# Optimization experiments

Hardware: AMD Instinct MI355X
Metric: run time of the kernel (lower is better)

The kernel has to match this reference:

```python
import jax, jax.numpy as jnp
import numpy as np

G = 8192          # graphs in batch
A = 5             # num_agents (nodes per graph)
N = G * A         # total nodes
IN_CH = 29
HID = 64
HEADS = 8
D = HID * HEADS   # 512, node/graph feature dim
NOPT = 4
ADIM = 3


def _lin(key, fan_in, fan_out):
    return jax.random.normal(key, (fan_in, fan_out), jnp.float32) / np.sqrt(fan_in)


def setup_inputs() -> dict:
    key = jax.random.key(0)
    ks = jax.random.split(key, 40)
    # --- graph structure: G fully-connected 5-node graphs + self loops ---
    pairs = np.array([(i, j) for i in range(A) for j in range(A) if i != j])  # [20,2]
    base = (np.arange(G)[:, None] * A)
    src = (base + pairs[None, :, 0]).reshape(-1)
    dst = (base + pairs[None, :, 1]).reshape(-1)
    # GATConv adds self loops (fill_value=0.0 for edge_attr)
    loop = np.arange(N)
    edge_src = jnp.asarray(np.concatenate([src, loop]), jnp.int32)
    edge_dst = jnp.asarray(np.concatenate([dst, loop]), jnp.int32)
    e_real = jax.random.uniform(ks[0], (src.shape[0], 1), jnp.float32)
    edge_attr = jnp.concatenate([e_real, jnp.zeros((N, 1), jnp.float32)], axis=0)
    batch_map = jnp.asarray(np.repeat(np.arange(G), A), jnp.int32)
    x = jax.random.normal(ks[1], (N, IN_CH), jnp.float32)
    sc = 1.0 / np.sqrt(HID)
    inp = dict(
        x=x, edge_attr=edge_attr, edge_src=edge_src, edge_dst=edge_dst, batch_map=batch_map,
        # conv1
        W1=_lin(ks[2], IN_CH, D), as1=jax.random.normal(ks[3], (HEADS, HID)) * sc,
        ad1=jax.random.normal(ks[4], (HEADS, HID)) * sc, We1=_lin(ks[5], 1, D),
        ae1=jax.random.normal(ks[6], (HEADS, HID)) * sc, b1=jnp.zeros((D,), jnp.float32),
        # conv2
        W2=_lin(ks[7], D, D), as2=jax.random.normal(ks[8], (HEADS, HID)) * sc,
        ad2=jax.random.normal(ks[9], (HEADS, HID)) * sc, We2=_lin(ks[10], 1, D),
        ae2=jax.random.normal(ks[11], (HEADS, HID)) * sc, b2=jnp.zeros((D,), jnp.float32),
        # policy-over-options head
        pw1=_lin(ks[12], D, 2 * HID), pb1=jnp.zeros((2 * HID,)), pw2=_lin(ks[13], 2 * HID, NOPT), pb2=jnp.zeros((NOPT,)),
        # q-options head
        qw1=_lin(ks[14], D, 2 * HID), qb1=jnp.zeros((2 * HID,)), qw2=_lin(ks[15], 2 * HID, NOPT), qb2=jnp.zeros((NOPT,)),
        # intra-option actor head (option 0), input dim = node + graph feature = 2*D
        aw1=_lin(ks[16], 2 * D, 2 * HID), ab1=jnp.zeros((2 * HID,)), aw2=_lin(ks[17], 2 * HID, 2 * ADIM), ab2=jnp.zeros((2 * ADIM,)),
        # termination head (option 0)
        tw1=_lin(ks[18], D, HID), tb1=jnp.zeros((HID,)), tw2=_lin(ks[19], HID, 1), tb2=jnp.zeros((1,)),
        action_limits=jnp.array([1.0, 1.0, 3.14159], jnp.float32),
    )
    return inp


def _gat(x, src, dst, eattr, W, a_s, a_d, We, a_e, b):
    n = x.shape[0]
    h = (x @ W).reshape(n, HEADS, HID)                      # [N,H,C]
    e = (eattr @ We).reshape(-1, HEADS, HID)                # [E,H,C]
    lg = ((h * a_s).sum(-1)[src] + (h * a_d).sum(-1)[dst]
          + (e * a_e).sum(-1))                              # [E,H]
    lg = jnp.where(lg > 0, lg, 0.2 * lg)                    # leaky_relu(0.2)
    m = jax.ops.segment_max(lg, dst, num_segments=n)
    p = jnp.exp(lg - m[dst])
    denom = jax.ops.segment_sum(p, dst, num_segments=n)[dst] + 1e-16
    alpha = p / denom                                       # scatter-softmax over dst
    out = jax.ops.segment_sum(alpha[:, :, None] * h[src], dst, num_segments=n)
    return out.reshape(n, HEADS * HID) + b


def reference(x, edge_attr, edge_src, edge_dst, batch_map,
              W1, as1, ad1, We1, ae1, b1,
              W2, as2, ad2, We2, ae2, b2,
              pw1, pb1, pw2, pb2, qw1, qb1, qw2, qb2,
              aw1, ab1, aw2, ab2, tw1, tb1, tw2, tb2, action_limits):
    h = jax.nn.relu(_gat(x, edge_src, edge_dst, edge_attr, W1, as1, ad1, We1, ae1, b1))
    h = jax.nn.relu(_gat(h, edge_src, edge_dst, edge_attr, W2, as2, ad2, We2, ae2, b2))
    # global_mean_pool
    cnt = jax.ops.segment_sum(jnp.ones((h.shape[0],), h.dtype), batch_map, num_segments=G)
    g = jax.ops.segment_sum(h, batch_map, num_segments=G) / cnt[:, None]   # [G,D]
    pi = jax.nn.relu(g @ pw1 + pb1) @ pw2 + pb2                            # [G,NOPT]
    q = jax.nn.relu(g @ qw1 + qb1) @ qw2 + qb2                             # [G,NOPT]
    term = jax.nn.sigmoid(jax.nn.relu(g @ tw1 + tb1) @ tw2 + tb2)          # [G,1]
    # per-graph first num_agents nodes == all nodes here (5 per graph)
    agent = h.reshape(G, A, D)
    comb = jnp.concatenate([agent, jnp.broadcast_to(g[:, None, :], (G, A, D))], axis=-1)
    ho = jax.nn.relu(comb @ aw1 + ab1) @ aw2 + ab2                          # [G,A,6]
    mean_raw, log_std_raw = jnp.split(ho, 2, axis=-1)
    mean = jnp.tanh(mean_raw) * action_limits                               # [G,A,3]
    std = 0.05 + jax.nn.sigmoid(log_std_raw) * 0.45 + 1e-6
    return jnp.concatenate([pi, q, term, mean.reshape(G, -1), std.reshape(G, -1)], axis=1)
```

## Files before the change

### kernel.cpp

```cpp
#include <hip/hip_runtime.h>
#include <hip/hip_bf16.h>
#include <math.h>

#define GG 8192
#define AA 5
#define NN (GG * AA)
#define DD 512

typedef unsigned short ushort_t;
typedef unsigned int uint_t;

__device__ inline float bf2f(ushort_t u) {
  union { uint_t i; float f; } c; c.i = ((uint_t)u) << 16; return c.f;
}
__device__ inline ushort_t f2bf(float f) {
  union { float f; uint_t i; } c; c.f = f;
  uint_t r = c.i + 0x7fffu + ((c.i >> 16) & 1u);
  return (ushort_t)(r >> 16);
}

using frag8 = __attribute__((ext_vector_type(8))) short;
using f32x4 = __attribute__((ext_vector_type(4))) float;

typedef __attribute__((address_space(3))) void lds_void;
typedef __attribute__((address_space(1))) const void gbl_void;
#define GLL(g, l) __builtin_amdgcn_global_load_lds((gbl_void*)(g), (lds_void*)(l), 16, 0, 0)

__device__ inline int xcd_swz(int bid, int nwg) {
  return (bid & 7) * (nwg >> 3) + (bid >> 3);
}

__global__ __launch_bounds__(256) void k_prep(
    const float* __restrict__ x, const float* __restrict__ W1,
    const float* __restrict__ W2, const float* __restrict__ pw1,
    const float* __restrict__ qw1, const float* __restrict__ tw1,
    const float* __restrict__ aw1, const float* __restrict__ pb1,
    const float* __restrict__ qb1, const float* __restrict__ tb1,
    const float* __restrict__ ab1, const float* __restrict__ We1,
    const float* __restrict__ ae1, const float* __restrict__ We2,
    const float* __restrict__ ae2, const float* __restrict__ as1,
    const float* __restrict__ ad1, const float* __restrict__ as2,
    const float* __restrict__ ad2, const float* __restrict__ pw2,
    const float* __restrict__ pb2, const float* __restrict__ qw2,
    const float* __restrict__ qb2, const float* __restrict__ tw2,
    const float* __restrict__ tb2, const float* __restrict__ aw2,
    const float* __restrict__ ab2, ushort_t* __restrict__ xpad32,
    ushort_t* __restrict__ W1T32, ushort_t* __restrict__ W2T,
    ushort_t* __restrict__ WcatT, ushort_t* __restrict__ aw1topT,
    ushort_t* __restrict__ wsc1T, ushort_t* __restrict__ wsc2T,
    float* __restrict__ bcat, float* __restrict__ sce,
    float* __restrict__ woutT, float* __restrict__ bout) {
  int b = blockIdx.x;
  int t = threadIdx.x;
  if (b < 1024) {
    int i = b * 256 + t;
    int n = i >> 9, k = i & 511;
    W2T[(size_t)n * 512 + k] = f2bf(W2[(size_t)k * 512 + n]);
    float v;
    if (n < 128)      v = pw1[(size_t)k * 128 + n];
    else if (n < 256) v = qw1[(size_t)k * 128 + (n - 128)];
    else if (n < 320) v = tw1[(size_t)k * 64 + (n - 256)];
    else if (n < 448) v = aw1[(size_t)(512 + k) * 128 + (n - 320)];
    else              v = 0.f;
    WcatT[(size_t)n * 512 + k] = f2bf(v);
    if (n < 128) aw1topT[(size_t)n * 512 + k] = f2bf(aw1[(size_t)k * 128 + n]);
    if (k == 0) {
      float bv;
      if (n < 128)      bv = pb1[n];
      else if (n < 256) bv = qb1[n - 128];
      else if (n < 320) bv = tb1[n - 256];
      else if (n < 448) bv = ab1[n - 320];
      else              bv = 0.f;
      bcat[n] = bv;
    }
    if (i < 512 * 32) {
      int nn = i >> 5, kk = i & 31;
      W1T32[i] = (kk < 29) ? f2bf(W1[(size_t)kk * 512 + nn]) : (ushort_t)0;
    }
    if (i < 16384) {
      int k2 = i & 511, srow = i >> 9;
      int nh2 = srow >> 4, s = srow & 15;
      float val = 0.f;
      if (s < 8) {
        int head = nh2 * 4 + (s >> 1);
        const float* av = ((s & 1) ? ad2 : as2) + head * 64;
        const float* wr = W2 + (size_t)k2 * 512 + head * 64;
        for (int c = 0; c < 64; ++c) val = fmaf(wr[c], av[c], val);
      }
      wsc2T[i] = f2bf(val);
    }
    if (i < 1024) {
      int k1 = i & 31, srow = i >> 5;
      int nh1 = srow >> 4, s = srow & 15;
      float val = 0.f;
      if (s < 8 && k1 < 29) {
        int head = nh1 * 4 + (s >> 1);
        const float* av = ((s & 1) ? ad1 : as1) + head * 64;
        const float* wr = W1 + (size_t)k1 * 512 + head * 64;
        for (int c = 0; c < 64; ++c) val = fmaf(wr[c], av[c], val);
      }
      wsc1T[i] = f2bf(val);
    }
    if (i < 16) {
      int h = i & 7;
      const float* Wp = (i < 8) ? We1 : We2;
      const float* ap = (i < 8) ? ae1 : ae2;
      float c = 0.f;
      for (int k2 = 0; k2 < 64; ++k2) c = fmaf(Wp[h * 64 + k2], ap[h * 64 + k2], c);
      sce[i] = c;
    }
    if (i < 5120) {
      int j = i / 40, o = i % 40;
      float wv;
      if (o < 4)       wv = pw2[j * 4 + o];
      else if (o < 8)  wv = qw2[j * 4 + (o - 4)];
      else if (o == 8) wv = (j < 64) ? tw2[j] : 0.f;
      else if (o < 24) wv = aw2[j * 6 + (o - 9) % 3];
      else if (o < 39) wv = aw2[j * 6 + 3 + (o - 24) % 3];
      else             wv = 0.f;
      woutT[i] = wv;
      if (j == 0) {
        float bv;
        if (o < 4)       bv = pb2[o];
        else if (o < 8)  bv = qb2[o - 4];
        else if (o == 8) bv = tb2[0];
        else if (o < 24) bv = ab2[(o - 9) % 3];
        else if (o < 39) bv = ab2[3 + (o - 24) % 3];
        else             bv = 0.f;
        bout[o] = bv;
      }
    }
  } else {
    int i = (b - 1024) * 256 + t;
    int n = i >> 5, k = i & 31;
    xpad32[i] = (k < 29) ? f2bf(x[(size_t)n * 29 + k]) : (ushort_t)0;
  }
}

template <int KDIM, bool POOL>
__global__ __launch_bounds__(512) void k_fused(
    const ushort_t* __restrict__ A, const ushort_t* __restrict__ BT,
    const ushort_t* __restrict__ WS, const float* __restrict__ eattr,
    const float* __restrict__ sce, const float* __restrict__ bvec,
    ushort_t* __restrict__ hout, ushort_t* __restrict__ gmean) {
  __shared__ __align__(16) char smem[51200];
  const int t = threadIdx.x;
  const int lane = t & 63;
  const int w = t >> 6;
  const int l15 = lane & 15;
  const int ko2 = ((((lane >> 4) ^ (lane & 3) ^ ((lane >> 2) & 3)) & 3) * 16);
  int lid = xcd_swz(blockIdx.x, gridDim.x);
  const int mb = lid >> 1, nh = lid & 1;
  const int m0 = mb * 80;
  const int g0 = mb * 16;
  const int n0 = nh * 256;
  const ushort_t* WSn = WS + (size_t)nh * 16 * KDIM;
  constexpr int nt = KDIM / 32;
  f32x4 acc[5][2] = {};
  f32x4 asc[5] = {};
  float* sal = (float*)(smem + 42240);
  float* sss = (float*)(smem + 48640);
  float* ssd = (float*)(smem + 49920);
#define FSTAGE(bi, kk0)                                                        \
  {                                                                            \
    char* bb_ = smem + (bi) * 16384;                                           \
    char* aa_ = smem + 32768 + (bi) * 5120;                                    \
    char* sb_ = smem + 43008 + (bi) * 1024;                                    \
    _Pragma("unroll")                                                          \
    for (int r_ = 0; r_ < 2; ++r_) {                                           \
      int c_ = t + r_ * 512; int row_ = c_ >> 2;                               \
      int sw_ = ((((c_ & 3) ^ (row_ & 3) ^ ((row_ >> 2) & 3)) & 3)) * 8;       \
      GLL(BT + (size_t)(n0 + row_) * KDIM + (kk0) + sw_, bb_ + c_ * 16);       \
    }                                                                          \
    if (t < 320) {                                                             \
      int c_ = t; int row_ = c_ >> 2;                                          \
      int sw_ = ((((c_ & 3) ^ (row_ & 3) ^ ((row_ >> 2) & 3)) & 3)) * 8;       \
      GLL(A + (size_t)(m0 + row_) * KDIM + (kk0) + sw_, aa_ + c_ * 16);        \
    } else if (t < 384) {                                                      \
      int c_ = t - 320; int row_ = c_ >> 2;                                    \
      int sw_ = ((((c_ & 3) ^ (row_ & 3) ^ ((row_ >> 2) & 3)) & 3)) * 8;       \
      GLL(WSn + (size_t)row_ * KDIM + (kk0) + sw_, sb_ + c_ * 16);             \
    }                                                                          \
  }
  FSTAGE(0, 0);
  for (int ts = 0; ts < nt; ++ts) {
    int cur = ts & 1;
    if (ts + 1 < nt) {
      FSTAGE(cur ^ 1, (ts + 1) * 32);
      if (w < 6) { asm volatile("s_waitcnt vmcnt(3)" ::: "memory"); }
      else       { asm volatile("s_waitcnt vmcnt(2)" ::: "memory"); }
    } else {
      asm volatile("s_waitcnt vmcnt(0)" ::: "memory");
    }
    __builtin_amdgcn_s_barrier();
    __builtin_amdgcn_sched_barrier(0);
    const char* bb = smem + cur * 16384;
    const char* aa = smem + 32768 + cur * 5120;
    const char* sb = smem + 43008 + cur * 1024;
    frag8 af[5], bfr[2];
#pragma unroll
    for (int mt = 0; mt < 5; ++mt)
      af[mt] = *(const frag8*)(aa + (mt * 16 + l15) * 64 + ko2);
#pragma unroll
    for (int n = 0; n < 2; ++n)
      bfr[n] = *(const frag8*)(bb + ((2 * w + n) * 16 + l15) * 64 + ko2);
    __builtin_amdgcn_s_setprio(1);
#pragma unroll
    for (int mt = 0; mt < 5; ++mt)
#pragma unroll
      for (int n = 0; n < 2; ++n)
        acc[mt][n] = __builtin_amdgcn_mfma_f32_16x16x32_bf16(af[mt], bfr[n], acc[mt][n], 0, 0, 0);
    if (w == 7) {
      frag8 sfr = *(const frag8*)(sb + l15 * 64 + ko2);
#pragma unroll
      for (int mt = 0; mt < 5; ++mt)
        asc[mt] = __builtin_amdgcn_mfma_f32_16x16x32_bf16(af[mt], sfr, asc[mt], 0, 0, 0);
    }
    __builtin_amdgcn_s_setprio(0);
    __builtin_amdgcn_sched_barrier(0);
    if (ts == nt - 1 && w == 7 && l15 < 8) {
      float* dst = (lane & 1) ? ssd : sss;
      int hd = l15 >> 1;
      int q4 = (lane >> 4) * 4;
#pragma unroll
      for (int mt = 0; mt < 5; ++mt)
#pragma unroll
        for (int r = 0; r < 4; ++r)
          dst[(mt * 16 + q4 + r) * 4 + hd] = asc[mt][r];
    }
    __builtin_amdgcn_s_barrier();
  }
#undef FSTAGE
  float* hbf = (float*)smem;
  {
    if (w < 4) {
      int q4 = (lane >> 4) * 4;
#pragma unroll
      for (int mt = 0; mt < 5; ++mt)
#pragma unroll
        for (int n = 0; n < 2; ++n) {
          int lc = w * 32 + n * 16 + l15;
#pragma unroll
          for (int r = 0; r < 4; ++r)
            hbf[(mt * 16 + q4 + r) * 132 + lc] = acc[mt][n][r];
        }
    } else if (t - 256 < 160) {
      int u = t - 256;
      int gi = u / 10, jh = u % 10;
      int j = jh >> 1, hd0 = jh & 1;
#pragma unroll
      for (int hh = 0; hh < 2; ++hh) {
        int hd = hd0 + hh * 2;
        int g = g0 + gi;
        float sdj = ssd[(gi * 5 + j) * 4 + hd];
        float ce = sce[nh * 4 + hd];
        float lg[5], mx = -1e30f;
#pragma unroll
        for (int i = 0; i < 5; ++i) {
          float l = sss[(gi * 5 + i) * 4 + hd] + sdj;
          if (i != j) l = fmaf(eattr[(size_t)g * 20 + i * 4 + (j > i ? j - 1 : j)], ce, l);
          l = l > 0.f ? l : 0.2f * l;
          lg[i] = l; mx = fmaxf(mx, l);
        }
        float s = 0.f;
#pragma unroll
        for (int i = 0; i < 5; ++i) { lg[i] = __expf(lg[i] - mx); s += lg[i]; }
        float inv = 1.f / (s + 1e-16f);
#pragma unroll
        for (int i = 0; i < 5; ++i) sal[((gi * 5 + j) * 5 + i) * 4 + hd] = lg[i] * inv;
      }
    }
  }
  __syncthreads();
#pragma unroll
  for (int half = 0; half < 2; ++half) {
    if (half == 1) {
      if (w >= 4) {
        int q4 = (lane >> 4) * 4;
#pragma unroll
        for (int mt = 0; mt < 5; ++mt)
#pragma unroll
          for (int n = 0; n < 2; ++n) {
            int lc = (w - 4) * 32 + n * 16 + l15;
#pragma unroll
            for (int r = 0; r < 4; ++r)
              hbf[(mt * 16 + q4 + r) * 132 + lc] = acc[mt][n][r];
          }
      }
      __syncthreads();
    }
    int gi = t >> 5, cq = t & 31;
    int hd = half * 2 + (cq >> 4);
    int colg = n0 + half * 128 + cq * 4;
    float hv[5][4];
#pragma unroll
    for (int i = 0; i < 5; ++i)
      *(float4*)hv[i] = *(const float4*)&hbf[(gi * 5 + i) * 132 + cq * 4];
    float4 bb4 = *(const float4*)&bvec[colg];
    float gs0 = 0.f, gs1 = 0.f, gs2 = 0.f, gs3 = 0.f;
#pragma unroll
    for (int j = 0; j < 5; ++j) {
      float o0 = bb4.x, o1 = bb4.y, o2 = bb4.z, o3 = bb4.w;
#pragma unroll
      for (int i = 0; i < 5; ++i) {
        float a = sal[((gi * 5 + j) * 5 + i) * 4 + hd];
        o0 = fmaf(a, hv[i][0], o0); o1 = fmaf(a, hv[i][1], o1);
        o2 = fmaf(a, hv[i][2], o2); o3 = fmaf(a, hv[i][3], o3);
      }
      o0 = fmaxf(o0, 0.f); o1 = fmaxf(o1, 0.f);
      o2 = fmaxf(o2, 0.f); o3 = fmaxf(o3, 0.f);
      uint2 wv_;
      wv_.x = (uint_t)f2bf(o0) | ((uint_t)f2bf(o1) << 16);
      wv_.y = (uint_t)f2bf(o2) | ((uint_t)f2bf(o3) << 16);
      *(uint2*)(hout + ((size_t)(g0 + gi) * 5 + j) * 512 + colg) = wv_;
      if (POOL) { gs0 += o0; gs1 += o1; gs2 += o2; gs3 += o3; }
    }
    if (POOL) {
      uint2 wv_;
      wv_.x = (uint_t)f2bf(gs0 * 0.2f) | ((uint_t)f2bf(gs1 * 0.2f) << 16);
      wv_.y = (uint_t)f2bf(gs2 * 0.2f) | ((uint_t)f2bf(gs3 * 0.2f) << 16);
      *(uint2*)(gmean + (size_t)(g0 + gi) * 512 + colg) = wv_;
    }
    if (half == 0) __syncthreads();
  }
}

template <int EPI>
__device__ __forceinline__ void gemm_body(
    const ushort_t* __restrict__ A, const ushort_t* __restrict__ BT,
    const float* __restrict__ bias, void* __restrict__ Cv,
    int M, int N, int K, int m0, int n0, char* lds) {
  int t = threadIdx.x;
  int lane = t & 63;
  int wv = t >> 6;
  int wr = (wv >> 1) * 64, wc = (wv & 1) * 64;
  f32x4 acc[4][4] = {};
  int ch0 = t, ch1 = t + 256;
  int row0 = ch0 >> 2, row1 = ch1 >> 2;
  int sw0 = (((ch0 & 3) ^ (row0 & 3) ^ ((row0 >> 2) & 3)) & 3) * 8;
  int sw1 = (((ch1 & 3) ^ (row1 & 3) ^ ((row1 >> 2) & 3)) & 3) * 8;
  int ko2 = ((((lane >> 4) ^ (lane & 3) ^ ((lane >> 2) & 3)) & 3) * 16);
  const int nt = K >> 5;
#define STAGE(bi, kk0)                                                         \
  {                                                                            \
    char* ab = lds + (bi) * 16384;                                             \
    GLL(A + (size_t)(m0 + row0) * K + (kk0) + sw0, ab + ch0 * 16);             \
    GLL(A + (size_t)(m0 + row1) * K + (kk0) + sw1, ab + ch1 * 16);             \
    GLL(BT + (size_t)(n0 + row0) * K + (kk0) + sw0, ab + 8192 + ch0 * 16);     \
    GLL(BT + (size_t)(n0 + row1) * K + (kk0) + sw1, ab + 8192 + ch1 * 16);     \
  }
  STAGE(0, 0);
  if (nt > 1) STAGE(1, 32);
  for (int ts = 0; ts < nt; ++ts) {
    int bi = ts % 3;
    if (ts + 2 < nt) {
      STAGE((ts + 2) % 3, (ts + 2) * 32);
      asm volatile("s_waitcnt vmcnt(8)" ::: "memory");
    } else if (ts + 1 < nt) {
      asm volatile("s_waitcnt vmcnt(4)" ::: "memory");
    } else {
      asm volatile("s_waitcnt vmcnt(0)" ::: "memory");
    }
    __builtin_amdgcn_s_barrier();
    __builtin_amdgcn_sched_barrier(0);
    const char* ab = lds + bi * 16384;
    frag8 af[4], bfr[4];
#pragma unroll
    for (int m = 0; m < 4; ++m)
      af[m] = *(const frag8*)(ab + (wr + m * 16 + (lane & 15)) * 64 + ko2);
#pragma unroll
    for (int n = 0; n < 4; ++n)
      bfr[n] = *(const frag8*)(ab + 8192 + (wc + n * 16 + (lane & 15)) * 64 + ko2);
#pragma unroll
    for (int m = 0; m < 4; ++m)
#pragma unroll
      for (int n = 0; n < 4; ++n)
        acc[m][n] = __builtin_amdgcn_mfma_f32_16x16x32_bf16(af[m], bfr[n], acc[m][n], 0, 0, 0);
    __builtin_amdgcn_sched_barrier(0);
    __builtin_amdgcn_s_barrier();
  }
#undef STAGE
  int r4 = (lane >> 4) * 4;
  int cl = lane & 15;
#pragma unroll
  for (int m = 0; m < 4; ++m) {
#pragma unroll
    for (int n = 0; n < 4; ++n) {
      int col = n0 + wc + n * 16 + cl;
      float bb = (EPI == 2) ? bias[col] : 0.f;
#pragma unroll
      for (int r = 0; r < 4; ++r) {
        int row = m0 + wr + m * 16 + r4 + r;
        float v = acc[m][n][r] + bb;
        if (EPI == 2 && col < 320) v = fmaxf(v, 0.f);
        ((float*)Cv)[(size_t)row * N + col] = v;
      }
    }
  }
}

__global__ __launch_bounds__(256) void k_hgemm(
    const ushort_t* __restrict__ h2, const ushort_t* __restrict__ aw1topT,
    float* __restrict__ ahid, const ushort_t* __restrict__ gmean,
    const ushort_t* __restrict__ WcatT, const float* __restrict__ bcat,
    float* __restrict__ hcat) {
  __shared__ char lds[49152];
  int bid = blockIdx.x;
  if (bid < 320) {
    int lid = xcd_swz(bid, 320);
    gemm_body<1>(h2, aw1topT, nullptr, ahid, NN, 128, DD, lid * 128, 0, lds);
  } else {
    int lid = xcd_swz(bid - 320, 256);
    gemm_body<2>(gmean, WcatT, bcat, hcat, GG, DD, DD, (lid >> 2) * 128, (lid & 3) * 128, lds);
  }
}

__global__ __launch_bounds__(256) void k_heads(
    const float* __restrict__ hcat, const float* __restrict__ ahid,
    const float* __restrict__ woutT, const float* __restrict__ bout,
    const float* __restrict__ alim, float* __restrict__ out) {
  int g0 = blockIdx.x * 4;
  int t = threadIdx.x;
  __shared__ float sbuf[4224];
  for (int i = t; i < 4224; i += 256) {
    int gi = i / 1056, r = i - gi * 1056;
    const float* grow = hcat + (size_t)(g0 + gi) * 512;
    float v = 0.f;
    if (r < 128)                  v = grow[r];
    else if (r >= 132 && r < 260) v = grow[128 + r - 132];
    else if (r >= 264 && r < 328) v = grow[256 + r - 264];
    else if (r >= 396) {
      int q = r - 396; int a = q / 132; int j = q - a * 132;
      if (j < 128)
        v = fmaxf(ahid[((size_t)(g0 + gi) * 5 + a) * 128 + j] + grow[320 + j], 0.f);
    }
    sbuf[i] = v;
  }
  __syncthreads();
  int gi = t >> 6, o = t & 63;
  int oc = o < 39 ? o : 39;
  int seg;
  if (oc < 4)       seg = 0;
  else if (oc < 8)  seg = 132;
  else if (oc == 8) seg = 264;
  else {
    int idx = (oc < 24) ? oc - 9 : oc - 24;
    seg = 396 + (idx / 3) * 132;
  }
  const float* ip = &sbuf[gi * 1056 + seg];
  float a0 = 0.f, a1 = 0.f, a2 = 0.f, a3 = 0.f;
#pragma unroll
  for (int j = 0; j < 128; j += 4) {
    a0 = fmaf(ip[j + 0], woutT[(j + 0) * 40 + oc], a0);
    a1 = fmaf(ip[j + 1], woutT[(j + 1) * 40 + oc], a1);
    a2 = fmaf(ip[j + 2], woutT[(j + 2) * 40 + oc], a2);
    a3 = fmaf(ip[j + 3], woutT[(j + 3) * 40 + oc], a3);
  }
  float res = (a0 + a1) + (a2 + a3) + bout[oc];
  if (o < 39) {
    if (o == 8)       res = 1.f / (1.f + __expf(-res));
    else if (o >= 24) res = 0.05f + 0.45f / (1.f + __expf(-res)) + 1e-6f;
    else if (o >= 9)  res = tanhf(res) * alim[(o - 9) % 3];
    out[(size_t)(g0 + gi) * 39 + o] = res;
  }
}

extern "C" void kernel_launch(void* const* d_in, const int* in_sizes, int n_in,
                              void* d_out, int out_size, void* d_ws, size_t ws_size,
                              hipStream_t stream) {
  const float* x     = (const float*)d_in[0];
  const float* eattr = (const float*)d_in[1];
  const float* W1  = (const float*)d_in[5];
  const float* as1 = (const float*)d_in[6];
  const float* ad1 = (const float*)d_in[7];
  const float* We1 = (const float*)d_in[8];
  const float* ae1 = (const float*)d_in[9];
  const float* b1  = (const float*)d_in[10];
  const float* W2  = (const float*)d_in[11];
  const float* as2 = (const float*)d_in[12];
  const float* ad2 = (const float*)d_in[13];
  const float* We2 = (const float*)d_in[14];
  const float* ae2 = (const float*)d_in[15];
  const float* b2  = (const float*)d_in[16];
  const float* pw1 = (const float*)d_in[17];
  const float* pb1 = (const float*)d_in[18];
  const float* pw2 = (const float*)d_in[19];
  const float* pb2 = (const float*)d_in[20];
  const float* qw1 = (const float*)d_in[21];
  const float* qb1 = (const float*)d_in[22];
  const float* qw2 = (const float*)d_in[23];
  const float* qb2 = (const float*)d_in[24];
  const float* aw1 = (const float*)d_in[25];
  const float* ab1 = (const float*)d_in[26];
  const float* aw2 = (const float*)d_in[27];
  const float* ab2 = (const float*)d_in[28];
  const float* tw1 = (const float*)d_in[29];
  const float* tb1 = (const float*)d_in[30];
  const float* tw2 = (const float*)d_in[31];
  const float* tb2 = (const float*)d_in[32];
  const float* alim = (const float*)d_in[33];

  const size_t BIGE = (size_t)NN * DD;
  char* p = (char*)d_ws;
  ushort_t* h1     = (ushort_t*)p; p += BIGE * 2;
  ushort_t* h2     = (ushort_t*)p; p += BIGE * 2;
  ushort_t* gmean  = (ushort_t*)p; p += (size_t)GG * DD * 2;
  ushort_t* xpad32 = (ushort_t*)p; p += (size_t)NN * 32 * 2;
  ushort_t* W1T32  = (ushort_t*)p; p += (size_t)512 * 32 * 2;
  ushort_t* W2T    = (ushort_t*)p; p += (size_t)512 * 512 * 2;
  ushort_t* WcatT  = (ushort_t*)p; p += (size_t)512 * 512 * 2;
  ushort_t* aw1topT = (ushort_t*)p; p += (size_t)128 * 512 * 2;
  ushort_t* wsc1T  = (ushort_t*)p; p += (size_t)2 * 16 * 32 * 2;
  ushort_t* wsc2T  = (ushort_t*)p; p += (size_t)2 * 16 * 512 * 2;
  float* bcat  = (float*)p; p += 512 * 4;
  float* sce   = (float*)p; p += 16 * 4;
  float* woutT = (float*)p; p += 5120 * 4;
  float* bout  = (float*)p; p += 40 * 4;
  float* ahid  = (float*)p; p += (size_t)NN * 128 * 4;
  float* hcat  = (float*)p;

  k_prep<<<1024 + 5120, 256, 0, stream>>>(
      x, W1, W2, pw1, qw1, tw1, aw1, pb1, qb1, tb1, ab1,
      We1, ae1, We2, ae2, as1, ad1, as2, ad2,
      pw2, pb2, qw2, qb2, tw2, tb2, aw2, ab2,
      xpad32, W1T32, W2T, WcatT, aw1topT, wsc1T, wsc2T,
      bcat, sce, woutT, bout);
  k_fused<32, false><<<(NN / 80) * 2, 512, 0, stream>>>(
      xpad32, W1T32, wsc1T, eattr, sce, b1, h1, nullptr);
  k_fused<512, true><<<(NN / 80) * 2, 512, 0, stream>>>(
      h1, W2T, wsc2T, eattr, sce + 8, b2, h2, gmean);
  k_hgemm<<<320 + 256, 256, 0, stream>>>(h2, aw1topT, ahid, gmean, WcatT, bcat, hcat);
  k_heads<<<GG / 4, 256, 0, stream>>>(hcat, ahid, woutT, bout, alim, (float*)d_out);
}
```

Measured before the change: 113.8 us.

## Fuse both GAT layers into one kernel keeping h1 in shared memory

```diff
diff --git a/kernel.cpp b/kernel.cpp
--- a/kernel.cpp
+++ b/kernel.cpp
@@ -77,24 +77,20 @@
       int nn = i >> 5, kk = i & 31;
       W1T32[i] = (kk < 29) ? f2bf(W1[(size_t)kk * 512 + nn]) : (ushort_t)0;
     }
-    if (i < 16384) {
-      int k2 = i & 511, srow = i >> 9;
-      int nh2 = srow >> 4, s = srow & 15;
+    if (i < 8192) {
+      int k2 = i & 511, s = i >> 9;
+      int head = s >> 1;
+      const float* av = ((s & 1) ? ad2 : as2) + head * 64;
+      const float* wr = W2 + (size_t)k2 * 512 + head * 64;
       float val = 0.f;
-      if (s < 8) {
-        int head = nh2 * 4 + (s >> 1);
-        const float* av = ((s & 1) ? ad2 : as2) + head * 64;
-        const float* wr = W2 + (size_t)k2 * 512 + head * 64;
-        for (int c = 0; c < 64; ++c) val = fmaf(wr[c], av[c], val);
-      }
+      for (int c = 0; c < 64; ++c) val = fmaf(wr[c], av[c], val);
       wsc2T[i] = f2bf(val);
     }
-    if (i < 1024) {
-      int k1 = i & 31, srow = i >> 5;
-      int nh1 = srow >> 4, s = srow & 15;
+    if (i < 512) {
+      int k1 = i & 31, s = i >> 5;
+      int head = s >> 1;
       float val = 0.f;
-      if (s < 8 && k1 < 29) {
-        int head = nh1 * 4 + (s >> 1);
+      if (k1 < 29) {
         const float* av = ((s & 1) ? ad1 : as1) + head * 64;
         const float* wr = W1 + (size_t)k1 * 512 + head * 64;
         for (int c = 0; c < 64; ++c) val = fmaf(wr[c], av[c], val);
@@ -137,66 +133,54 @@
   }
 }
 
-template <int KDIM, bool POOL>
-__global__ __launch_bounds__(512) void k_fused(
-    const ushort_t* __restrict__ A, const ushort_t* __restrict__ BT,
-    const ushort_t* __restrict__ WS, const float* __restrict__ eattr,
-    const float* __restrict__ sce, const float* __restrict__ bvec,
-    ushort_t* __restrict__ hout, ushort_t* __restrict__ gmean) {
-  __shared__ __align__(16) char smem[51200];
+__global__ __launch_bounds__(1024) void k_mega(
+    const ushort_t* __restrict__ xpad32, const ushort_t* __restrict__ W1T32,
+    const ushort_t* __restrict__ wsc1T, const ushort_t* __restrict__ W2T,
+    const ushort_t* __restrict__ wsc2T, const float* __restrict__ eattr,
+    const float* __restrict__ sce, const float* __restrict__ b1,
+    const float* __restrict__ b2, ushort_t* __restrict__ h2,
+    ushort_t* __restrict__ gmean) {
+  __shared__ __align__(16) char smem[149504];
   const int t = threadIdx.x;
   const int lane = t & 63;
   const int w = t >> 6;
   const int l15 = lane & 15;
   const int ko2 = ((((lane >> 4) ^ (lane & 3) ^ ((lane >> 2) & 3)) & 3) * 16);
   int lid = xcd_swz(blockIdx.x, gridDim.x);
-  const int mb = lid >> 1, nh = lid & 1;
-  const int m0 = mb * 80;
-  const int g0 = mb * 16;
-  const int n0 = nh * 256;
-  const ushort_t* WSn = WS + (size_t)nh * 16 * KDIM;
-  constexpr int nt = KDIM / 32;
-  f32x4 acc[5][2] = {};
-  f32x4 asc[5] = {};
-  float* sal = (float*)(smem + 42240);
-  float* sss = (float*)(smem + 48640);
-  float* ssd = (float*)(smem + 49920);
-#define FSTAGE(bi, kk0)                                                        \
-  {                                                                            \
-    char* bb_ = smem + (bi) * 16384;                                           \
-    char* aa_ = smem + 32768 + (bi) * 5120;                                    \
-    char* sb_ = smem + 43008 + (bi) * 1024;                                    \
-    _Pragma("unroll")                                                          \
-    for (int r_ = 0; r_ < 2; ++r_) {                                           \
-      int c_ = t + r_ * 512; int row_ = c_ >> 2;                               \
-      int sw_ = ((((c_ & 3) ^ (row_ & 3) ^ ((row_ >> 2) & 3)) & 3)) * 8;       \
-      GLL(BT + (size_t)(n0 + row_) * KDIM + (kk0) + sw_, bb_ + c_ * 16);       \
-    }                                                                          \
-    if (t < 320) {                                                             \
-      int c_ = t; int row_ = c_ >> 2;                                          \
-      int sw_ = ((((c_ & 3) ^ (row_ & 3) ^ ((row_ >> 2) & 3)) & 3)) * 8;       \
-      GLL(A + (size_t)(m0 + row_) * KDIM + (kk0) + sw_, aa_ + c_ * 16);        \
-    } else if (t < 384) {                                                      \
-      int c_ = t - 320; int row_ = c_ >> 2;                                    \
-      int sw_ = ((((c_ & 3) ^ (row_ & 3) ^ ((row_ >> 2) & 3)) & 3)) * 8;       \
-      GLL(WSn + (size_t)row_ * KDIM + (kk0) + sw_, sb_ + c_ * 16);             \
-    }                                                                          \
-  }
-  FSTAGE(0, 0);
-  for (int ts = 0; ts < nt; ++ts) {
-    int cur = ts & 1;
-    if (ts + 1 < nt) {
-      FSTAGE(cur ^ 1, (ts + 1) * 32);
-      if (w < 6) { asm volatile("s_waitcnt vmcnt(3)" ::: "memory"); }
-      else       { asm volatile("s_waitcnt vmcnt(2)" ::: "memory"); }
-    } else {
-      asm volatile("s_waitcnt vmcnt(0)" ::: "memory");
-    }
-    __builtin_amdgcn_s_barrier();
-    __builtin_amdgcn_sched_barrier(0);
-    const char* bb = smem + cur * 16384;
-    const char* aa = smem + 32768 + cur * 5120;
-    const char* sb = smem + 43008 + cur * 1024;
+  const int m0 = lid * 80;
+  const int g0 = lid * 16;
+  ushort_t* h1buf = (ushort_t*)smem;
+  float* sal = (float*)(smem + 124160);
+  float* sss = (float*)(smem + 136960);
+  float* ssd = (float*)(smem + 139520);
+  const f32x4 zz = {0.f, 0.f, 0.f, 0.f};
+  f32x4 acc[5][2], asc[5];
+#pragma unroll
+  for (int mt = 0; mt < 5; ++mt) { acc[mt][0] = zz; acc[mt][1] = zz; asc[mt] = zz; }
+
+  {
+#pragma unroll
+    for (int r_ = 0; r_ < 2; ++r_) {
+      int c_ = t + r_ * 1024; int row_ = c_ >> 2;
+      int sw_ = ((((c_ & 3) ^ (row_ & 3) ^ ((row_ >> 2) & 3)) & 3)) * 8;
+      GLL(W1T32 + (size_t)row_ * 32 + sw_, smem + 81920 + c_ * 16);
+    }
+    if (t < 320) {
+      int c_ = t; int row_ = c_ >> 2;
+      int sw_ = ((((c_ & 3) ^ (row_ & 3) ^ ((row_ >> 2) & 3)) & 3)) * 8;
+      GLL(xpad32 + (size_t)(m0 + row_) * 32 + sw_, smem + 114688 + c_ * 16);
+    } else if (t < 384) {
+      int c_ = t - 320; int row_ = c_ >> 2;
+      int sw_ = ((((c_ & 3) ^ (row_ & 3) ^ ((row_ >> 2) & 3)) & 3)) * 8;
+      GLL(wsc1T + (size_t)row_ * 32 + sw_, smem + 119808 + c_ * 16);
+    }
+  }
+  asm volatile("s_waitcnt vmcnt(0)" ::: "memory");
+  __builtin_amdgcn_s_barrier();
+  {
+    const char* bb = smem + 81920;
+    const char* aa = smem + 114688;
+    const char* sb = smem + 119808;
     frag8 af[5], bfr[2];
 #pragma unroll
     for (int mt = 0; mt < 5; ++mt)
@@ -204,124 +188,242 @@
 #pragma unroll
     for (int n = 0; n < 2; ++n)
       bfr[n] = *(const frag8*)(bb + ((2 * w + n) * 16 + l15) * 64 + ko2);
-    __builtin_amdgcn_s_setprio(1);
 #pragma unroll
     for (int mt = 0; mt < 5; ++mt)
 #pragma unroll
       for (int n = 0; n < 2; ++n)
         acc[mt][n] = __builtin_amdgcn_mfma_f32_16x16x32_bf16(af[mt], bfr[n], acc[mt][n], 0, 0, 0);
-    if (w == 7) {
+    if (w == 15) {
       frag8 sfr = *(const frag8*)(sb + l15 * 64 + ko2);
 #pragma unroll
       for (int mt = 0; mt < 5; ++mt)
         asc[mt] = __builtin_amdgcn_mfma_f32_16x16x32_bf16(af[mt], sfr, asc[mt], 0, 0, 0);
     }
-    __builtin_amdgcn_s_setprio(0);
-    __builtin_amdgcn_sched_barrier(0);
-    if (ts == nt - 1 && w == 7 && l15 < 8) {
-      float* dst = (lane & 1) ? ssd : sss;
-      int hd = l15 >> 1;
-      int q4 = (lane >> 4) * 4;
-#pragma unroll
-      for (int mt = 0; mt < 5; ++mt)
-#pragma unroll
-        for (int r = 0; r < 4; ++r)
-          dst[(mt * 16 + q4 + r) * 4 + hd] = asc[mt][r];
-    }
-    __builtin_amdgcn_s_barrier();
-  }
-#undef FSTAGE
-  float* hbf = (float*)smem;
+  }
+  if (w == 15) {
+    float* dst = (l15 & 1) ? ssd : sss;
+    int hd = l15 >> 1;
+    int q4 = (lane >> 4) * 4;
+#pragma unroll
+    for (int mt = 0; mt < 5; ++mt)
+#pragma unroll
+      for (int r = 0; r < 4; ++r)
+        dst[(mt * 16 + q4 + r) * 8 + hd] = asc[mt][r];
+  }
+  __syncthreads();
+  if (t < 640) {
+    int gi = t / 40, jh = t % 40;
+    int j = jh >> 3, hd = jh & 7;
+    int g = g0 + gi;
+    float sdj = ssd[(gi * 5 + j) * 8 + hd];
+    float ce = sce[hd];
+    float lg[5], mx = -1e30f;
+#pragma unroll
+    for (int i = 0; i < 5; ++i) {
+      float l = sss[(gi * 5 + i) * 8 + hd] + sdj;
+      if (i != j) l = fmaf(eattr[(size_t)g * 20 + i * 4 + (j > i ? j - 1 : j)], ce, l);
+      l = l > 0.f ? l : 0.2f * l;
+      lg[i] = l; mx = fmaxf(mx, l);
+    }
+    float s = 0.f;
+#pragma unroll
+    for (int i = 0; i < 5; ++i) { lg[i] = __expf(lg[i] - mx); s += lg[i]; }
+    float inv = 1.f / (s + 1e-16f);
+#pragma unroll
+    for (int i = 0; i < 5; ++i) sal[((gi * 5 + j) * 5 + i) * 8 + hd] = lg[i] * inv;
+  }
+  __syncthreads();
   {
-    if (w < 4) {
-      int q4 = (lane >> 4) * 4;
-#pragma unroll
-      for (int mt = 0; mt < 5; ++mt)
-#pragma unroll
-        for (int n = 0; n < 2; ++n) {
-          int lc = w * 32 + n * 16 + l15;
-#pragma unroll
-          for (int r = 0; r < 4; ++r)
-            hbf[(mt * 16 + q4 + r) * 132 + lc] = acc[mt][n][r];
-        }
-    } else if (t - 256 < 160) {
-      int u = t - 256;
-      int gi = u / 10, jh = u % 10;
-      int j = jh >> 1, hd0 = jh & 1;
-#pragma unroll
-      for (int hh = 0; hh < 2; ++hh) {
-        int hd = hd0 + hh * 2;
-        int g = g0 + gi;
-        float sdj = ssd[(gi * 5 + j) * 4 + hd];
-        float ce = sce[nh * 4 + hd];
-        float lg[5], mx = -1e30f;
-#pragma unroll
-        for (int i = 0; i < 5; ++i) {
-          float l = sss[(gi * 5 + i) * 4 + hd] + sdj;
-          if (i != j) l = fmaf(eattr[(size_t)g * 20 + i * 4 + (j > i ? j - 1 : j)], ce, l);
-          l = l > 0.f ? l : 0.2f * l;
-          lg[i] = l; mx = fmaxf(mx, l);
-        }
-        float s = 0.f;
-#pragma unroll
-        for (int i = 0; i < 5; ++i) { lg[i] = __expf(lg[i] - mx); s += lg[i]; }
-        float inv = 1.f / (s + 1e-16f);
-#pragma unroll
-        for (int i = 0; i < 5; ++i) sal[((gi * 5 + j) * 5 + i) * 4 + hd] = lg[i] * inv;
-      }
-    }
-  }
-  __syncthreads();
-#pragma unroll
-  for (int half = 0; half < 2; ++half) {
-    if (half == 1) {
-      if (w >= 4) {
+    float* hbf = (float*)(smem + 81920);
+#pragma unroll
+    for (int p = 0; p < 4; ++p) {
+      if ((w >> 2) == p) {
         int q4 = (lane >> 4) * 4;
 #pragma unroll
         for (int mt = 0; mt < 5; ++mt)
 #pragma unroll
           for (int n = 0; n < 2; ++n) {
-            int lc = (w - 4) * 32 + n * 16 + l15;
+            int lc = (w & 3) * 32 + n * 16 + l15;
 #pragma unroll
             for (int r = 0; r < 4; ++r)
               hbf[(mt * 16 + q4 + r) * 132 + lc] = acc[mt][n][r];
           }
       }
       __syncthreads();
-    }
-    int gi = t >> 5, cq = t & 31;
-    int hd = half * 2 + (cq >> 4);
-    int colg = n0 + half * 128 + cq * 4;
-    float hv[5][4];
-#pragma unroll
-    for (int i = 0; i < 5; ++i)
-      *(float4*)hv[i] = *(const float4*)&hbf[(gi * 5 + i) * 132 + cq * 4];
-    float4 bb4 = *(const float4*)&bvec[colg];
-    float gs0 = 0.f, gs1 = 0.f, gs2 = 0.f, gs3 = 0.f;
-#pragma unroll
-    for (int j = 0; j < 5; ++j) {
-      float o0 = bb4.x, o1 = bb4.y, o2 = bb4.z, o3 = bb4.w;
-#pragma unroll
-      for (int i = 0; i < 5; ++i) {
-        float a = sal[((gi * 5 + j) * 5 + i) * 4 + hd];
-        o0 = fmaf(a, hv[i][0], o0); o1 = fmaf(a, hv[i][1], o1);
-        o2 = fmaf(a, hv[i][2], o2); o3 = fmaf(a, hv[i][3], o3);
+      if (t < 512) {
+        int gi = t >> 5, cq = t & 31;
+        int hd = 2 * p + (cq >> 4);
+        int cg = p * 128 + cq * 4;
+        float hv[5][4];
+#pragma unroll
+        for (int i = 0; i < 5; ++i)
+          *(float4*)hv[i] = *(const float4*)&hbf[(gi * 5 + i) * 132 + cq * 4];
+        float4 bb4 = *(const float4*)&b1[cg];
+        int chunk = cg >> 5, slot = (cg >> 3) & 3, boff = (cg & 7) * 2;
+#pragma unroll
+        for (int j = 0; j < 5; ++j) {
+          float o0 = bb4.x, o1 = bb4.y, o2 = bb4.z, o3 = bb4.w;
+#pragma unroll
+          for (int i = 0; i < 5; ++i) {
+            float a = sal[((gi * 5 + j) * 5 + i) * 8 + hd];
+            o0 = fmaf(a, hv[i][0], o0); o1 = fmaf(a, hv[i][1], o1);
+            o2 = fmaf(a, hv[i][2], o2); o3 = fmaf(a, hv[i][3], o3);
+          }
+          o0 = fmaxf(o0, 0.f); o1 = fmaxf(o1, 0.f);
+          o2 = fmaxf(o2, 0.f); o3 = fmaxf(o3, 0.f);
+          uint2 wv_;
+          wv_.x = (uint_t)f2bf(o0) | ((uint_t)f2bf(o1) << 16);
+          wv_.y = (uint_t)f2bf(o2) | ((uint_t)f2bf(o3) << 16);
+          int row = gi * 5 + j;
+          int phys = slot ^ (row & 3) ^ ((row >> 2) & 3);
+          *(uint2*)((char*)h1buf + chunk * 5120 + row * 64 + phys * 16 + boff) = wv_;
+        }
       }
-      o0 = fmaxf(o0, 0.f); o1 = fmaxf(o1, 0.f);
-      o2 = fmaxf(o2, 0.f); o3 = fmaxf(o3, 0.f);
-      uint2 wv_;
-      wv_.x = (uint_t)f2bf(o0) | ((uint_t)f2bf(o1) << 16);
-      wv_.y = (uint_t)f2bf(o2) | ((uint_t)f2bf(o3) << 16);
-      *(uint2*)(hout + ((size_t)(g0 + gi) * 5 + j) * 512 + colg) = wv_;
-      if (POOL) { gs0 += o0; gs1 += o1; gs2 += o2; gs3 += o3; }
-    }
-    if (POOL) {
-      uint2 wv_;
-      wv_.x = (uint_t)f2bf(gs0 * 0.2f) | ((uint_t)f2bf(gs1 * 0.2f) << 16);
-      wv_.y = (uint_t)f2bf(gs2 * 0.2f) | ((uint_t)f2bf(gs3 * 0.2f) << 16);
-      *(uint2*)(gmean + (size_t)(g0 + gi) * 512 + colg) = wv_;
-    }
-    if (half == 0) __syncthreads();
+      __syncthreads();
+    }
+  }
+
+#pragma unroll
+  for (int mt = 0; mt < 5; ++mt) { acc[mt][0] = zz; acc[mt][1] = zz; asc[mt] = zz; }
+#define FS2(bi, kk0)                                                           \
+  {                                                                            \
+    char* bb_ = smem + 81920 + (bi) * 32768;                                   \
+    char* sb_ = smem + 147456 + (bi) * 1024;                                   \
+    _Pragma("unroll")                                                          \
+    for (int r_ = 0; r_ < 2; ++r_) {                                           \
+      int c_ = t + r_ * 1024; int row_ = c_ >> 2;                              \
+      int sw_ = ((((c_ & 3) ^ (row_ & 3) ^ ((row_ >> 2) & 3)) & 3)) * 8;       \
+      GLL(W2T + (size_t)row_ * 512 + (kk0) + sw_, bb_ + c_ * 16);              \
+    }                                                                          \
+    if (t < 64) {                                                              \
+      int c_ = t; int row_ = c_ >> 2;                                          \
+      int sw_ = ((((c_ & 3) ^ (row_ & 3) ^ ((row_ >> 2) & 3)) & 3)) * 8;       \
+      GLL(wsc2T + (size_t)row_ * 512 + (kk0) + sw_, sb_ + c_ * 16);            \
+    }                                                                          \
+  }
+  FS2(0, 0);
+  for (int ts = 0; ts < 16; ++ts) {
+    int cur = ts & 1;
+    if (ts + 1 < 16) {
+      FS2(cur ^ 1, (ts + 1) * 32);
+      if (w == 0) { asm volatile("s_waitcnt vmcnt(3)" ::: "memory"); }
+      else        { asm volatile("s_waitcnt vmcnt(2)" ::: "memory"); }
+    } else {
+      asm volatile("s_waitcnt vmcnt(0)" ::: "memory");
+    }
+    __builtin_amdgcn_s_barrier();
+    __builtin_amdgcn_sched_barrier(0);
+    const char* bb = smem + 81920 + cur * 32768;
+    const char* aa = (const char*)h1buf + ts * 5120;
+    const char* sb = smem + 147456 + cur * 1024;
+    frag8 af[5], bfr[2];
+#pragma unroll
+    for (int mt = 0; mt < 5; ++mt)
+      af[mt] = *(const frag8*)(aa + (mt * 16 + l15) * 64 + ko2);
+#pragma unroll
+    for (int n = 0; n < 2; ++n)
+      bfr[n] = *(const frag8*)(bb + ((2 * w + n) * 16 + l15) * 64 + ko2);
+    __builtin_amdgcn_s_setprio(1);
+#pragma unroll
+    for (int mt = 0; mt < 5; ++mt)
+#pragma unroll
+      for (int n = 0; n < 2; ++n)
+        acc[mt][n] = __builtin_amdgcn_mfma_f32_16x16x32_bf16(af[mt], bfr[n], acc[mt][n], 0, 0, 0);
+    if (w == 15) {
+      frag8 sfr = *(const frag8*)(sb + l15 * 64 + ko2);
+#pragma unroll
+      for (int mt = 0; mt < 5; ++mt)
+        asc[mt] = __builtin_amdgcn_mfma_f32_16x16x32_bf16(af[mt], sfr, asc[mt], 0, 0, 0);
+    }
+    __builtin_amdgcn_s_setprio(0);
+    __builtin_amdgcn_sched_barrier(0);
+    __builtin_amdgcn_s_barrier();
+  }
+#undef FS2
+  if (w == 15) {
+    float* dst = (l15 & 1) ? ssd : sss;
+    int hd = l15 >> 1;
+    int q4 = (lane >> 4) * 4;
+#pragma unroll
+    for (int mt = 0; mt < 5; ++mt)
+#pragma unroll
+      for (int r = 0; r < 4; ++r)
+        dst[(mt * 16 + q4 + r) * 8 + hd] = asc[mt][r];
+  }
+  __syncthreads();
+  if (t < 640) {
+    int gi = t / 40, jh = t % 40;
+    int j = jh >> 3, hd = jh & 7;
+    int g = g0 + gi;
+    float sdj = ssd[(gi * 5 + j) * 8 + hd];
+    float ce = sce[8 + hd];
+    float lg[5], mx = -1e30f;
+#pragma unroll
+    for (int i = 0; i < 5; ++i) {
+      float l = sss[(gi * 5 + i) * 8 + hd] + sdj;
+      if (i != j) l = fmaf(eattr[(size_t)g * 20 + i * 4 + (j > i ? j - 1 : j)], ce, l);
+      l = l > 0.f ? l : 0.2f * l;
+      lg[i] = l; mx = fmaxf(mx, l);
+    }
+    float s = 0.f;
+#pragma unroll
+    for (int i = 0; i < 5; ++i) { lg[i] = __expf(lg[i] - mx); s += lg[i]; }
+    float inv = 1.f / (s + 1e-16f);
+#pragma unroll
+    for (int i = 0; i < 5; ++i) sal[((gi * 5 + j) * 5 + i) * 8 + hd] = lg[i] * inv;
+  }
+  __syncthreads();
+  {
+    float* hbf = (float*)(smem + 81920);
+#pragma unroll
+    for (int p = 0; p < 4; ++p) {
+      if ((w >> 2) == p) {
+        int q4 = (lane >> 4) * 4;
+#pragma unroll
+        for (int mt = 0; mt < 5; ++mt)
+#pragma unroll
+          for (int n = 0; n < 2; ++n) {
+            int lc = (w & 3) * 32 + n * 16 + l15;
+#pragma unroll
+            for (int r = 0; r < 4; ++r)
+              hbf[(mt * 16 + q4 + r) * 132 + lc] = acc[mt][n][r];
+          }
+      }
+      __syncthreads();
+      if (t < 512) {
+        int gi = t >> 5, cq = t & 31;
+        int hd = 2 * p + (cq >> 4);
+        int cg = p * 128 + cq * 4;
+        float hv[5][4];
+#pragma unroll
+        for (int i = 0; i < 5; ++i)
+          *(float4*)hv[i] = *(const float4*)&hbf[(gi * 5 + i) * 132 + cq * 4];
+        float4 bb4 = *(const float4*)&b2[cg];
+        float gs0 = 0.f, gs1 = 0.f, gs2 = 0.f, gs3 = 0.f;
+#pragma unroll
+        for (int j = 0; j < 5; ++j) {
+          float o0 = bb4.x, o1 = bb4.y, o2 = bb4.z, o3 = bb4.w;
+#pragma unroll
+          for (int i = 0; i < 5; ++i) {
+            float a = sal[((gi * 5 + j) * 5 + i) * 8 + hd];
+            o0 = fmaf(a, hv[i][0], o0); o1 = fmaf(a, hv[i][1], o1);
+            o2 = fmaf(a, hv[i][2], o2); o3 = fmaf(a, hv[i][3], o3);
+          }
+          o0 = fmaxf(o0, 0.f); o1 = fmaxf(o1, 0.f);
+          o2 = fmaxf(o2, 0.f); o3 = fmaxf(o3, 0.f);
+          uint2 wv_;
+          wv_.x = (uint_t)f2bf(o0) | ((uint_t)f2bf(o1) << 16);
+          wv_.y = (uint_t)f2bf(o2) | ((uint_t)f2bf(o3) << 16);
+          *(uint2*)(h2 + ((size_t)(g0 + gi) * 5 + j) * 512 + cg) = wv_;
+          gs0 += o0; gs1 += o1; gs2 += o2; gs3 += o3;
+        }
+        uint2 wv_;
+        wv_.x = (uint_t)f2bf(gs0 * 0.2f) | ((uint_t)f2bf(gs1 * 0.2f) << 16);
+        wv_.y = (uint_t)f2bf(gs2 * 0.2f) | ((uint_t)f2bf(gs3 * 0.2f) << 16);
+        *(uint2*)(gmean + (size_t)(g0 + gi) * 512 + cg) = wv_;
+      }
+      __syncthreads();
+    }
   }
 }
 
@@ -502,7 +604,6 @@
 
   const size_t BIGE = (size_t)NN * DD;
   char* p = (char*)d_ws;
-  ushort_t* h1     = (ushort_t*)p; p += BIGE * 2;
   ushort_t* h2     = (ushort_t*)p; p += BIGE * 2;
   ushort_t* gmean  = (ushort_t*)p; p += (size_t)GG * DD * 2;
   ushort_t* xpad32 = (ushort_t*)p; p += (size_t)NN * 32 * 2;
@@ -510,8 +611,8 @@
   ushort_t* W2T    = (ushort_t*)p; p += (size_t)512 * 512 * 2;
   ushort_t* WcatT  = (ushort_t*)p; p += (size_t)512 * 512 * 2;
   ushort_t* aw1topT = (ushort_t*)p; p += (size_t)128 * 512 * 2;
-  ushort_t* wsc1T  = (ushort_t*)p; p += (size_t)2 * 16 * 32 * 2;
-  ushort_t* wsc2T  = (ushort_t*)p; p += (size_t)2 * 16 * 512 * 2;
+  ushort_t* wsc1T  = (ushort_t*)p; p += (size_t)16 * 32 * 2;
+  ushort_t* wsc2T  = (ushort_t*)p; p += (size_t)16 * 512 * 2;
   float* bcat  = (float*)p; p += 512 * 4;
   float* sce   = (float*)p; p += 16 * 4;
   float* woutT = (float*)p; p += 5120 * 4;
@@ -525,10 +626,8 @@
       pw2, pb2, qw2, qb2, tw2, tb2, aw2, ab2,
       xpad32, W1T32, W2T, WcatT, aw1topT, wsc1T, wsc2T,
       bcat, sce, woutT, bout);
-  k_fused<32, false><<<(NN / 80) * 2, 512, 0, stream>>>(
-      xpad32, W1T32, wsc1T, eattr, sce, b1, h1, nullptr);
-  k_fused<512, true><<<(NN / 80) * 2, 512, 0, stream>>>(
-      h1, W2T, wsc2T, eattr, sce + 8, b2, h2, gmean);
+  k_mega<<<GG / 16, 1024, 0, stream>>>(
+      xpad32, W1T32, wsc1T, W2T, wsc2T, eattr, sce, b1, b2, h2, gmean);
   k_hgemm<<<320 + 256, 256, 0, stream>>>(h2, aw1topT, ahid, gmean, WcatT, bcat, hcat);
   k_heads<<<GG / 4, 256, 0, stream>>>(hcat, ahid, woutT, bout, alim, (float*)d_out);
 }
```

Result: no change. 111.9 us (-1.6%).
